# Optimization experiments

Hardware: AMD Instinct MI355X
Metric: run time of the kernel (lower is better)

The kernel has to match this reference:

```python
import jax, jax.numpy as jnp
import numpy as np

B, T, D, H, E = 4, 2048, 1024, 4096, 8


def setup_inputs() -> dict:
    key = jax.random.key(0)
    ks = jax.random.split(key, 7)
    x = jax.random.normal(ks[0], (B, T, D), dtype=jnp.float32)
    # Gate: Linear(D, E)
    Wg = jax.random.normal(ks[1], (D, E), dtype=jnp.float32) / np.sqrt(D)
    bg = jax.random.normal(ks[2], (E,), dtype=jnp.float32) * 0.01
    # Experts: E x [Linear(D,H), ReLU, Linear(H,D)] (dropout inactive at eval)
    W1 = jax.random.normal(ks[3], (E, D, H), dtype=jnp.float32) / np.sqrt(D)
    b1 = jax.random.normal(ks[4], (E, H), dtype=jnp.float32) * 0.01
    W2 = jax.random.normal(ks[5], (E, H, D), dtype=jnp.float32) / np.sqrt(H)
    b2 = jax.random.normal(ks[6], (E, D), dtype=jnp.float32) * 0.01
    return {"x": x, "Wg": Wg, "bg": bg, "W1": W1, "b1": b1, "W2": W2, "b2": b2}


def reference(x, Wg, bg, W1, b1, W2, b2):
    # Gate + hard top-1 routing
    gate_scores = x @ Wg + bg                      # [B,T,E]
    top1 = jnp.argmax(gate_scores, axis=-1)        # [B,T]
    onehot = jax.nn.one_hot(top1, Wg.shape[-1], dtype=x.dtype)  # [B,T,E]
    # Dense: every expert MLP over all tokens (matches original's masked
    # formulation: x*mask == x on selected tokens, output re-masked).
    h = jax.nn.relu(jnp.einsum('btd,edh->beth', x, W1) + b1[None, :, None, :])
    y = jnp.einsum('beth,ehd->betd', h, W2) + b2[None, :, None, :]
    # Masked combine: keep only the token's chosen expert output
    out = jnp.einsum('betd,bte->btd', y, onehot)
    return out
```

## Files before the change

### kernel.cpp

```cpp
#include <hip/hip_runtime.h>
#include <hip/hip_bf16.h>
#include <stdint.h>

#define NTOK 8192
#define DDIM 1024
#define HDIM 4096
#define NEXP 8
#define MAXWL 48

typedef __attribute__((ext_vector_type(4))) float f32x4;
typedef __attribute__((ext_vector_type(8))) short s16x8;
typedef __attribute__((ext_vector_type(8))) unsigned short u16x8;

__device__ __forceinline__ unsigned short f2bf(float f) {
  union { float f; unsigned int u; } v; v.f = f;
  unsigned int u = v.u;
  u += 0x7FFFu + ((u >> 16) & 1u);
  return (unsigned short)(u >> 16);
}

typedef __attribute__((address_space(3))) unsigned char lds_u8;
typedef const __attribute__((address_space(1))) unsigned char glb_u8;

__device__ __forceinline__ void load_lds16(const void* g, void* l) {
  __builtin_amdgcn_global_load_lds((glb_u8*)g, (lds_u8*)l, 16, 0, 0);
}

__global__ __launch_bounds__(256) void gate_kernel(
    const float* __restrict__ x, const float* __restrict__ Wg,
    const float* __restrict__ bg, int* __restrict__ counts,
    int* __restrict__ lists) {
  const int lane = threadIdx.x & 63;
  const int tok = blockIdx.x * 4 + (threadIdx.x >> 6);
  const float* xr = x + (size_t)tok * DDIM;
  double acc[NEXP];
#pragma unroll
  for (int e = 0; e < NEXP; ++e) acc[e] = 0.0;
#pragma unroll 4
  for (int it = 0; it < DDIM / 64; ++it) {
    const int d = it * 64 + lane;
    const float xv = xr[d];
    const f32x4 w0 = *(const f32x4*)(Wg + (size_t)d * NEXP);
    const f32x4 w1 = *(const f32x4*)(Wg + (size_t)d * NEXP + 4);
#pragma unroll
    for (int j = 0; j < 4; ++j) {
      acc[j]     += (double)xv * (double)w0[j];
      acc[4 + j] += (double)xv * (double)w1[j];
    }
  }
#pragma unroll
  for (int e = 0; e < NEXP; ++e) {
    double v = acc[e];
#pragma unroll
    for (int off = 32; off > 0; off >>= 1) v += __shfl_xor(v, off, 64);
    acc[e] = v;
  }
  if (lane == 0) {
    int best = 0;
    double bv = acc[0] + (double)bg[0];
#pragma unroll
    for (int e = 1; e < NEXP; ++e) {
      const double v = acc[e] + (double)bg[e];
      if (v > bv) { bv = v; best = e; }
    }
    const int pos = atomicAdd(&counts[best], 1);
    lists[best * NTOK + pos] = tok;
  }
}

__global__ void offs_kernel(const int* __restrict__ counts, int* __restrict__ offs,
                            int* __restrict__ wl) {
  int s = 0;
#pragma unroll
  for (int e = 0; e < NEXP; ++e) { offs[e] = s; s += counts[e]; }
  offs[NEXP] = s;
  int n = 0;
  for (int e = 0; e < NEXP; ++e) {
    const int nb = (counts[e] + 255) >> 8;
    for (int b = 0; b < nb; ++b) wl[n++] = (e << 20) | b;
  }
  offs[NEXP + 1] = n;
}

__global__ __launch_bounds__(256) void gather_conv_kernel(
    const float* __restrict__ x, const int* __restrict__ offs,
    const int* __restrict__ lists, int* __restrict__ stok,
    unsigned short* __restrict__ xbs) {
  const int p = blockIdx.x * 4 + (threadIdx.x >> 6);
  const int lane = threadIdx.x & 63;
  int e = 0;
#pragma unroll
  for (int k = 1; k < NEXP; ++k) e += (p >= offs[k]) ? 1 : 0;
  const int tok = lists[e * NTOK + (p - offs[e])];
  if (lane == 0) stok[p] = tok;
  const float* src = x + (size_t)tok * DDIM + lane * 16;
  unsigned short* dst = xbs + (size_t)p * DDIM + lane * 16;
#pragma unroll
  for (int q = 0; q < 2; ++q) {
    const f32x4 a = *(const f32x4*)(src + q * 8);
    const f32x4 b = *(const f32x4*)(src + q * 8 + 4);
    u16x8 o;
#pragma unroll
    for (int j = 0; j < 4; ++j) { o[j] = f2bf(a[j]); o[4 + j] = f2bf(b[j]); }
    *(u16x8*)(dst + q * 8) = o;
  }
}

__global__ __launch_bounds__(256) void transpose_conv_kernel(
    const float* __restrict__ in, unsigned short* __restrict__ out,
    int R, int C) {
  __shared__ unsigned short T[64][66];
  const int e = blockIdx.z;
  const float* ine = in + (size_t)e * R * C;
  unsigned short* oute = out + (size_t)e * C * R;
  const int c0 = blockIdx.x * 64, r0 = blockIdx.y * 64;
  const int t = threadIdx.x;
  const int tr = t >> 4, tc4 = (t & 15) * 4;
#pragma unroll
  for (int p = 0; p < 4; ++p) {
    const int r = tr + p * 16;
    const f32x4 v = *(const f32x4*)(ine + (size_t)(r0 + r) * C + c0 + tc4);
#pragma unroll
    for (int j = 0; j < 4; ++j) T[r][tc4 + j] = f2bf(v[j]);
  }
  __syncthreads();
  const int cc = t >> 3, rr8 = (t & 7) * 8;
#pragma unroll
  for (int p = 0; p < 2; ++p) {
    const int c = cc + p * 32;
    u16x8 o;
#pragma unroll
    for (int j = 0; j < 8; ++j) o[j] = T[rr8 + j][c];
    *(u16x8*)(oute + (size_t)(c0 + c) * R + r0 + rr8) = o;
  }
}

template <int BM, int BN, int WM, int WN, int K, int N, bool FUSE1>
__global__ __launch_bounds__(64 * WM * WN, 2) void ffn_kernel(
    const unsigned short* __restrict__ A, const unsigned short* __restrict__ Bt,
    const float* __restrict__ bias, const int* __restrict__ counts,
    const int* __restrict__ offs, const int* __restrict__ wl,
    const int* __restrict__ stok, unsigned short* __restrict__ outb,
    float* __restrict__ outf) {
  constexpr int MF = BM / (WM * 16);
  constexpr int NF = BN / (WN * 16);
  constexpr int ISS_A = BM / 64;
  constexpr int ISS_B = BN / 64;
  constexpr int NT = K / 64;
  constexpr int NCB = N / BN;
  constexpr int NWG = NCB * MAXWL;
  static_assert((NWG & 7) == 0 && (NT & 1) == 0 && NT >= 4, "");

  const int d = blockIdx.x;
  const int logical = (d & 7) * (NWG / 8) + (d >> 3);
  const int col0 = (logical / MAXWL) * BN;
  const int wli = logical % MAXWL;
  if (wli >= offs[NEXP + 1]) return;
  const int wle = wl[wli];
  const int e = wle >> 20;
  const int bx = wle & 0xFFFFF;
  const int cnt = counts[e];
  const int row0 = offs[e] + bx * BM;

  __shared__ __align__(16) unsigned short As0[BM * 64], Bs0[BN * 64];
  __shared__ __align__(16) unsigned short As1[BM * 64], Bs1[BN * 64];

  const int tid = threadIdx.x;
  const int lane = tid & 63;
  const int w = tid >> 6;
  const int wm = w / WN;
  const int wn = w % WN;
  const int fr = lane & 15;
  const int fj = lane >> 4;

  const int swz = ((tid & 7) ^ ((tid >> 3) & 7)) * 8;
  const int rb = tid >> 3;
  const unsigned short* srcA[ISS_A];
#pragma unroll
  for (int i = 0; i < ISS_A; ++i) {
    int gr = row0 + i * 64 + rb;
    if (gr > NTOK - 1) gr = NTOK - 1;
    srcA[i] = A + (size_t)gr * K + swz;
  }
  const unsigned short* Bte = Bt + (size_t)e * N * K;
  const unsigned short* srcB[ISS_B];
#pragma unroll
  for (int i = 0; i < ISS_B; ++i)
    srcB[i] = Bte + (size_t)(col0 + i * 64 + rb) * K + swz;

  f32x4 acc[MF][NF];
#pragma unroll
  for (int m = 0; m < MF; ++m)
#pragma unroll
    for (int n = 0; n < NF; ++n) acc[m][n] = f32x4{0.f, 0.f, 0.f, 0.f};

  auto stage = [&](unsigned short* dA, unsigned short* dB, int k0) {
#pragma unroll
    for (int i = 0; i < ISS_A; ++i)
      load_lds16(srcA[i] + k0, dA + i * 64 * 64 + tid * 8);
#pragma unroll
    for (int i = 0; i < ISS_B; ++i)
      load_lds16(srcB[i] + k0, dB + i * 64 * 64 + tid * 8);
  };

  auto compute = [&](const unsigned short* pA, const unsigned short* pB) {
#pragma unroll
    for (int kk = 0; kk < 2; ++kk) {
      const int js = (((kk << 2) + fj) ^ (fr & 7)) << 3;
      s16x8 af[MF], bf[NF];
#pragma unroll
      for (int m = 0; m < MF; ++m)
        af[m] = *(const s16x8*)(pA + (wm * MF * 16 + m * 16 + fr) * 64 + js);
#pragma unroll
      for (int n = 0; n < NF; ++n)
        bf[n] = *(const s16x8*)(pB + (wn * NF * 16 + n * 16 + fr) * 64 + js);
      __builtin_amdgcn_s_setprio(1);
#pragma unroll
      for (int m = 0; m < MF; ++m)
#pragma unroll
        for (int n = 0; n < NF; ++n)
          acc[m][n] = __builtin_amdgcn_mfma_f32_16x16x32_bf16(af[m], bf[n],
                                                              acc[m][n], 0, 0, 0);
      __builtin_amdgcn_s_setprio(0);
    }
  };

  stage(As0, Bs0, 0);
  asm volatile("s_waitcnt vmcnt(0)" ::: "memory");
  __builtin_amdgcn_s_barrier();

#pragma unroll 1
  for (int t = 0; t < NT - 2; t += 2) {
    stage(As1, Bs1, (t + 1) * 64);
    compute(As0, Bs0);
    asm volatile("s_waitcnt vmcnt(0)" ::: "memory");
    __builtin_amdgcn_s_barrier();
    stage(As0, Bs0, (t + 2) * 64);
    compute(As1, Bs1);
    asm volatile("s_waitcnt vmcnt(0)" ::: "memory");
    __builtin_amdgcn_s_barrier();
  }
  stage(As1, Bs1, (NT - 1) * 64);
  compute(As0, Bs0);
  asm volatile("s_waitcnt vmcnt(0)" ::: "memory");
  __builtin_amdgcn_s_barrier();
  compute(As1, Bs1);

#pragma unroll
  for (int n = 0; n < NF; ++n) {
    const int col = col0 + wn * NF * 16 + n * 16 + fr;
    const float bv = bias[e * N + col];
#pragma unroll
    for (int m = 0; m < MF; ++m) {
#pragma unroll
      for (int j = 0; j < 4; ++j) {
        const int rl = wm * MF * 16 + m * 16 + fj * 4 + j;
        if (bx * BM + rl < cnt) {
          if constexpr (FUSE1) {
            outb[(size_t)(row0 + rl) * N + col] = f2bf(fmaxf(acc[m][n][j] + bv, 0.f));
          } else {
            outf[(size_t)stok[row0 + rl] * N + col] = acc[m][n][j] + bv;
          }
        }
      }
    }
  }
}

extern "C" void kernel_launch(void* const* d_in, const int* in_sizes, int n_in,
                              void* d_out, int out_size, void* d_ws, size_t ws_size,
                              hipStream_t stream) {
  (void)in_sizes; (void)n_in; (void)out_size;
  const float* x  = (const float*)d_in[0];
  const float* Wg = (const float*)d_in[1];
  const float* bg = (const float*)d_in[2];
  const float* W1 = (const float*)d_in[3];
  const float* b1 = (const float*)d_in[4];
  const float* W2 = (const float*)d_in[5];
  const float* b2 = (const float*)d_in[6];
  float* out = (float*)d_out;

  char* ws = (char*)d_ws;
  const size_t OFF_CNT = 0;
  const size_t OFF_OFF = 128;
  const size_t OFF_WL  = 256;
  const size_t OFF_LST = 1024;
  const size_t OFF_STK = OFF_LST + (size_t)NEXP * NTOK * 4;
  const size_t OFF_XBS = OFF_STK + (size_t)NTOK * 4;
  const size_t OFF_HS  = OFF_XBS + (size_t)NTOK * DDIM * 2;
  const size_t OFF_WT  = OFF_HS + (size_t)NTOK * HDIM * 2;
  const size_t NEED    = OFF_WT + (size_t)NEXP * DDIM * HDIM * 2;
  if (ws_size < NEED) return;

  int* counts = (int*)(ws + OFF_CNT);
  int* offs   = (int*)(ws + OFF_OFF);
  int* wl     = (int*)(ws + OFF_WL);
  int* lists  = (int*)(ws + OFF_LST);
  int* stok   = (int*)(ws + OFF_STK);
  unsigned short* xbs = (unsigned short*)(ws + OFF_XBS);
  unsigned short* Hs  = (unsigned short*)(ws + OFF_HS);
  unsigned short* Wt  = (unsigned short*)(ws + OFF_WT);

  hipMemsetAsync(counts, 0, 128, stream);
  gate_kernel<<<NTOK / 4, 256, 0, stream>>>(x, Wg, bg, counts, lists);
  offs_kernel<<<1, 1, 0, stream>>>(counts, offs, wl);
  gather_conv_kernel<<<NTOK / 4, 256, 0, stream>>>(x, offs, lists, stok, xbs);

  transpose_conv_kernel<<<dim3(HDIM / 64, DDIM / 64, NEXP), 256, 0, stream>>>(
      W1, Wt, DDIM, HDIM);
  ffn_kernel<256, 256, 2, 4, DDIM, HDIM, true>
      <<<dim3((HDIM / 256) * MAXWL), 512, 0, stream>>>(
          xbs, Wt, b1, counts, offs, wl, stok, Hs, nullptr);
  transpose_conv_kernel<<<dim3(DDIM / 64, HDIM / 64, NEXP), 256, 0, stream>>>(
      W2, Wt, HDIM, DDIM);
  ffn_kernel<256, 128, 4, 2, HDIM, DDIM, false>
      <<<dim3((DDIM / 128) * MAXWL), 512, 0, stream>>>(
          Hs, Wt, b2, counts, offs, wl, stok, nullptr, out);
}
```

Measured before the change: 509.9 us.

## Halve K-step to 32, drop LDS swizzle, retile second FFN GEMM with separate worklist

The K tile per stage drops from 64 to 32, so each row is one 64-byte segment and the XOR swizzle is removed. The main loop now waits and barriers at the top of each step, before issuing the next prefetch. The second GEMM moves from 256x128 tiles to 128x256 tiles and gets its own worklist of 128-row blocks, which is meant to improve load balance across experts and cut partial-tile waste. The risks are more barriers per unit of work, possible LDS bank conflicts without the swizzle, and less overlap because each prefetch starts only after the barrier.

```diff
diff --git a/kernel.cpp b/kernel.cpp
--- a/kernel.cpp
+++ b/kernel.cpp
@@ -6,7 +6,8 @@
 #define DDIM 1024
 #define HDIM 4096
 #define NEXP 8
-#define MAXWL 48
+#define MAXWL1 48
+#define MAXWL2 72
 
 typedef __attribute__((ext_vector_type(4))) float f32x4;
 typedef __attribute__((ext_vector_type(8))) short s16x8;
@@ -69,17 +70,20 @@
 }
 
 __global__ void offs_kernel(const int* __restrict__ counts, int* __restrict__ offs,
-                            int* __restrict__ wl) {
+                            int* __restrict__ wl1, int* __restrict__ wl2) {
   int s = 0;
 #pragma unroll
   for (int e = 0; e < NEXP; ++e) { offs[e] = s; s += counts[e]; }
   offs[NEXP] = s;
-  int n = 0;
+  int n1 = 0, n2 = 0;
   for (int e = 0; e < NEXP; ++e) {
-    const int nb = (counts[e] + 255) >> 8;
-    for (int b = 0; b < nb; ++b) wl[n++] = (e << 20) | b;
-  }
-  offs[NEXP + 1] = n;
+    const int nb1 = (counts[e] + 255) >> 8;
+    for (int b = 0; b < nb1; ++b) wl1[n1++] = (e << 20) | b;
+    const int nb2 = (counts[e] + 127) >> 7;
+    for (int b = 0; b < nb2; ++b) wl2[n2++] = (e << 20) | b;
+  }
+  offs[NEXP + 1] = n1;
+  offs[NEXP + 2] = n2;
 }
 
 __global__ __launch_bounds__(256) void gather_conv_kernel(
@@ -135,35 +139,36 @@
   }
 }
 
-template <int BM, int BN, int WM, int WN, int K, int N, bool FUSE1>
-__global__ __launch_bounds__(64 * WM * WN, 2) void ffn_kernel(
+template <int BM, int BN, int WN, int K, int N, int MAXWLT, bool FUSE1>
+__global__ __launch_bounds__(512, 2) void ffn_kernel(
     const unsigned short* __restrict__ A, const unsigned short* __restrict__ Bt,
     const float* __restrict__ bias, const int* __restrict__ counts,
     const int* __restrict__ offs, const int* __restrict__ wl,
     const int* __restrict__ stok, unsigned short* __restrict__ outb,
-    float* __restrict__ outf) {
+    float* __restrict__ outf, int nwl_idx) {
+  constexpr int WM = 8 / WN;
   constexpr int MF = BM / (WM * 16);
   constexpr int NF = BN / (WN * 16);
-  constexpr int ISS_A = BM / 64;
-  constexpr int ISS_B = BN / 64;
-  constexpr int NT = K / 64;
+  constexpr int ISS_A = BM / 128;
+  constexpr int ISS_B = BN / 128;
+  constexpr int NT = K / 32;
   constexpr int NCB = N / BN;
-  constexpr int NWG = NCB * MAXWL;
+  constexpr int NWG = NCB * MAXWLT;
   static_assert((NWG & 7) == 0 && (NT & 1) == 0 && NT >= 4, "");
 
   const int d = blockIdx.x;
   const int logical = (d & 7) * (NWG / 8) + (d >> 3);
-  const int col0 = (logical / MAXWL) * BN;
-  const int wli = logical % MAXWL;
-  if (wli >= offs[NEXP + 1]) return;
+  const int col0 = (logical / MAXWLT) * BN;
+  const int wli = logical % MAXWLT;
+  if (wli >= offs[nwl_idx]) return;
   const int wle = wl[wli];
   const int e = wle >> 20;
   const int bx = wle & 0xFFFFF;
   const int cnt = counts[e];
   const int row0 = offs[e] + bx * BM;
 
-  __shared__ __align__(16) unsigned short As0[BM * 64], Bs0[BN * 64];
-  __shared__ __align__(16) unsigned short As1[BM * 64], Bs1[BN * 64];
+  __shared__ __align__(16) unsigned short As0[BM * 32], Bs0[BN * 32];
+  __shared__ __align__(16) unsigned short As1[BM * 32], Bs1[BN * 32];
 
   const int tid = threadIdx.x;
   const int lane = tid & 63;
@@ -173,20 +178,20 @@
   const int fr = lane & 15;
   const int fj = lane >> 4;
 
-  const int swz = ((tid & 7) ^ ((tid >> 3) & 7)) * 8;
-  const int rb = tid >> 3;
+  const int kslot = (tid & 3) * 8;
+  const int rb = tid >> 2;
   const unsigned short* srcA[ISS_A];
 #pragma unroll
   for (int i = 0; i < ISS_A; ++i) {
-    int gr = row0 + i * 64 + rb;
+    int gr = row0 + i * 128 + rb;
     if (gr > NTOK - 1) gr = NTOK - 1;
-    srcA[i] = A + (size_t)gr * K + swz;
+    srcA[i] = A + (size_t)gr * K + kslot;
   }
   const unsigned short* Bte = Bt + (size_t)e * N * K;
   const unsigned short* srcB[ISS_B];
 #pragma unroll
   for (int i = 0; i < ISS_B; ++i)
-    srcB[i] = Bte + (size_t)(col0 + i * 64 + rb) * K + swz;
+    srcB[i] = Bte + (size_t)(col0 + i * 128 + rb) * K + kslot;
 
   f32x4 acc[MF][NF];
 #pragma unroll
@@ -194,57 +199,47 @@
 #pragma unroll
     for (int n = 0; n < NF; ++n) acc[m][n] = f32x4{0.f, 0.f, 0.f, 0.f};
 
-  auto stage = [&](unsigned short* dA, unsigned short* dB, int k0) {
+  auto stage = [&](unsigned short* dA, unsigned short* dB, int kel) {
 #pragma unroll
     for (int i = 0; i < ISS_A; ++i)
-      load_lds16(srcA[i] + k0, dA + i * 64 * 64 + tid * 8);
+      load_lds16(srcA[i] + kel, dA + i * 128 * 32 + tid * 8);
 #pragma unroll
     for (int i = 0; i < ISS_B; ++i)
-      load_lds16(srcB[i] + k0, dB + i * 64 * 64 + tid * 8);
+      load_lds16(srcB[i] + kel, dB + i * 128 * 32 + tid * 8);
   };
 
-  auto compute = [&](const unsigned short* pA, const unsigned short* pB) {
-#pragma unroll
-    for (int kk = 0; kk < 2; ++kk) {
-      const int js = (((kk << 2) + fj) ^ (fr & 7)) << 3;
-      s16x8 af[MF], bf[NF];
-#pragma unroll
-      for (int m = 0; m < MF; ++m)
-        af[m] = *(const s16x8*)(pA + (wm * MF * 16 + m * 16 + fr) * 64 + js);
+  auto body = [&](const unsigned short* pA, const unsigned short* pB,
+                  unsigned short* nA, unsigned short* nB, int knext,
+                  bool do_stage) {
+    asm volatile("s_waitcnt vmcnt(0)" ::: "memory");
+    __builtin_amdgcn_s_barrier();
+    asm volatile("" ::: "memory");
+    if (do_stage) stage(nA, nB, knext);
+    s16x8 af[MF], bf[NF];
+#pragma unroll
+    for (int m = 0; m < MF; ++m)
+      af[m] = *(const s16x8*)(pA + (wm * MF * 16 + m * 16 + fr) * 32 + fj * 8);
+#pragma unroll
+    for (int n = 0; n < NF; ++n)
+      bf[n] = *(const s16x8*)(pB + (wn * NF * 16 + n * 16 + fr) * 32 + fj * 8);
+    __builtin_amdgcn_s_setprio(1);
+#pragma unroll
+    for (int m = 0; m < MF; ++m)
 #pragma unroll
       for (int n = 0; n < NF; ++n)
-        bf[n] = *(const s16x8*)(pB + (wn * NF * 16 + n * 16 + fr) * 64 + js);
-      __builtin_amdgcn_s_setprio(1);
-#pragma unroll
-      for (int m = 0; m < MF; ++m)
-#pragma unroll
-        for (int n = 0; n < NF; ++n)
-          acc[m][n] = __builtin_amdgcn_mfma_f32_16x16x32_bf16(af[m], bf[n],
-                                                              acc[m][n], 0, 0, 0);
-      __builtin_amdgcn_s_setprio(0);
-    }
+        acc[m][n] = __builtin_amdgcn_mfma_f32_16x16x32_bf16(af[m], bf[n],
+                                                            acc[m][n], 0, 0, 0);
+    __builtin_amdgcn_s_setprio(0);
   };
 
   stage(As0, Bs0, 0);
-  asm volatile("s_waitcnt vmcnt(0)" ::: "memory");
-  __builtin_amdgcn_s_barrier();
-
 #pragma unroll 1
   for (int t = 0; t < NT - 2; t += 2) {
-    stage(As1, Bs1, (t + 1) * 64);
-    compute(As0, Bs0);
-    asm volatile("s_waitcnt vmcnt(0)" ::: "memory");
-    __builtin_amdgcn_s_barrier();
-    stage(As0, Bs0, (t + 2) * 64);
-    compute(As1, Bs1);
-    asm volatile("s_waitcnt vmcnt(0)" ::: "memory");
-    __builtin_amdgcn_s_barrier();
-  }
-  stage(As1, Bs1, (NT - 1) * 64);
-  compute(As0, Bs0);
-  asm volatile("s_waitcnt vmcnt(0)" ::: "memory");
-  __builtin_amdgcn_s_barrier();
-  compute(As1, Bs1);
+    body(As0, Bs0, As1, Bs1, (t + 1) * 32, true);
+    body(As1, Bs1, As0, Bs0, (t + 2) * 32, true);
+  }
+  body(As0, Bs0, As1, Bs1, (NT - 1) * 32, true);
+  body(As1, Bs1, nullptr, nullptr, 0, false);
 
 #pragma unroll
   for (int n = 0; n < NF; ++n) {
@@ -283,7 +278,8 @@
   char* ws = (char*)d_ws;
   const size_t OFF_CNT = 0;
   const size_t OFF_OFF = 128;
-  const size_t OFF_WL  = 256;
+  const size_t OFF_WL1 = 256;
+  const size_t OFF_WL2 = 256 + MAXWL1 * 4;
   const size_t OFF_LST = 1024;
   const size_t OFF_STK = OFF_LST + (size_t)NEXP * NTOK * 4;
   const size_t OFF_XBS = OFF_STK + (size_t)NTOK * 4;
@@ -294,7 +290,8 @@
 
   int* counts = (int*)(ws + OFF_CNT);
   int* offs   = (int*)(ws + OFF_OFF);
-  int* wl     = (int*)(ws + OFF_WL);
+  int* wl1    = (int*)(ws + OFF_WL1);
+  int* wl2    = (int*)(ws + OFF_WL2);
   int* lists  = (int*)(ws + OFF_LST);
   int* stok   = (int*)(ws + OFF_STK);
   unsigned short* xbs = (unsigned short*)(ws + OFF_XBS);
@@ -303,17 +300,17 @@
 
   hipMemsetAsync(counts, 0, 128, stream);
   gate_kernel<<<NTOK / 4, 256, 0, stream>>>(x, Wg, bg, counts, lists);
-  offs_kernel<<<1, 1, 0, stream>>>(counts, offs, wl);
+  offs_kernel<<<1, 1, 0, stream>>>(counts, offs, wl1, wl2);
   gather_conv_kernel<<<NTOK / 4, 256, 0, stream>>>(x, offs, lists, stok, xbs);
 
   transpose_conv_kernel<<<dim3(HDIM / 64, DDIM / 64, NEXP), 256, 0, stream>>>(
       W1, Wt, DDIM, HDIM);
-  ffn_kernel<256, 256, 2, 4, DDIM, HDIM, true>
-      <<<dim3((HDIM / 256) * MAXWL), 512, 0, stream>>>(
-          xbs, Wt, b1, counts, offs, wl, stok, Hs, nullptr);
+  ffn_kernel<256, 256, 4, DDIM, HDIM, MAXWL1, true>
+      <<<dim3((HDIM / 256) * MAXWL1), 512, 0, stream>>>(
+          xbs, Wt, b1, counts, offs, wl1, stok, Hs, nullptr, NEXP + 1);
   transpose_conv_kernel<<<dim3(DDIM / 64, HDIM / 64, NEXP), 256, 0, stream>>>(
       W2, Wt, HDIM, DDIM);
-  ffn_kernel<256, 128, 4, 2, HDIM, DDIM, false>
-      <<<dim3((DDIM / 128) * MAXWL), 512, 0, stream>>>(
-          Hs, Wt, b2, counts, offs, wl, stok, nullptr, out);
-}
+  ffn_kernel<128, 256, 4, HDIM, DDIM, MAXWL2, false>
+      <<<dim3((DDIM / 256) * MAXWL2), 512, 0, stream>>>(
+          Hs, Wt, b2, counts, offs, wl2, stok, nullptr, out, NEXP + 2);
+}
```

Result: slower. 542.4 us (+6.4%).
